# Kernel optimization log

Hardware: AMD Instinct MI355X
Metric: run time of the kernel (lower is better)

Reference implementation:

```python
import jax, jax.numpy as jnp
import numpy as np

LOG_SQRT_2PI = 0.5 * float(np.log(2.0 * np.pi))  # 0.5*log(2*pi)


def _bayes_layer(x, mu, p, eps):
    # std_w = 1e-6 + softplus(W_p); W = W_mu + std_w * eps
    std = 1e-6 + jax.nn.softplus(p)
    W = mu + std * eps
    out = x @ W
    # variational posterior loglike q(W | mu, std), summed
    lqw = jnp.sum(-LOG_SQRT_2PI - jnp.log(std) - 0.5 * ((W - mu) / std) ** 2)
    # prior loglike N(0, 1) on detached W (original does W.detach().cpu().numpy())
    Wd = jax.lax.stop_gradient(W)
    lpw = jnp.sum(-LOG_SQRT_2PI - 0.5 * Wd ** 2)
    return out, lqw, lpw


def setup_inputs() -> dict:
    key = jax.random.key(0)
    ks = jax.random.split(key, 10)
    B, D_in, D_h, D_out = 65536, 512, 512, 10
    u = lambda k, s, lo, hi: jax.random.uniform(k, s, jnp.float32, lo, hi)
    return {
        "x": jax.random.normal(ks[0], (B, D_in), jnp.float32),
        "W_mu1": u(ks[1], (D_in, D_h), -0.2, 0.2),
        "W_p1": u(ks[2], (D_in, D_h), -3.0, -2.0),
        "eps1": jax.random.normal(ks[3], (D_in, D_h), jnp.float32),
        "W_mu2": u(ks[4], (D_h, D_h), -0.2, 0.2),
        "W_p2": u(ks[5], (D_h, D_h), -3.0, -2.0),
        "eps2": jax.random.normal(ks[6], (D_h, D_h), jnp.float32),
        "W_mu3": u(ks[7], (D_h, D_out), -0.2, 0.2),
        "W_p3": u(ks[8], (D_h, D_out), -3.0, -2.0),
        "eps3": jax.random.normal(ks[9], (D_h, D_out), jnp.float32),
    }


def reference(x, W_mu1, W_p1, eps1, W_mu2, W_p2, eps2, W_mu3, W_p3, eps3):
    # training / sample=True path of bayes_linear_2L.forward
    h, lqw1, lpw1 = _bayes_layer(x, W_mu1, W_p1, eps1)
    h = jax.nn.relu(h)
    h, lqw2, lpw2 = _bayes_layer(h, W_mu2, W_p2, eps2)
    h = jax.nn.relu(h)
    y, lqw3, lpw3 = _bayes_layer(h, W_mu3, W_p3, eps3)
    tlqw = lqw1 + lqw2 + lqw3
    tlpw = lpw1 + lpw2 + lpw3
    return (y, tlqw, tlpw)
```

## Files before the change

kernel.cpp:

```cpp
#include <hip/hip_runtime.h>
#include <hip/hip_bf16.h>
#include <stdint.h>

typedef unsigned char u8;
typedef unsigned int u32;
typedef unsigned long long u64;
typedef long i64;
typedef i64 i64x2 __attribute__((ext_vector_type(2)));
typedef float f32x4 __attribute__((ext_vector_type(4)));

#define LOGSQRT2PI 0.9189385332046727f
#define SB0() __builtin_amdgcn_sched_barrier(0)
#define MFMA8(A, B, C) __builtin_amdgcn_mfma_f32_16x16x32_fp8_fp8(A, B, C, 0, 0, 0)

__device__ __forceinline__ void gload_lds16(const void* g, void* l) {
    __builtin_amdgcn_global_load_lds((__attribute__((address_space(1))) void*)g,
                                     (__attribute__((address_space(3))) void*)l,
                                     16, 0, 0);
}

__device__ __forceinline__ u8 to_fp8(float v) {
    return (u8)(__builtin_amdgcn_cvt_pk_fp8_f32(v, 0.f, 0, false) & 0xff);
}

__device__ __forceinline__ i64x2 cvt_frag(const float* base) {
    float4 v0 = *(const float4*)(base);
    float4 v1 = *(const float4*)(base + 4);
    float4 v2 = *(const float4*)(base + 8);
    float4 v3 = *(const float4*)(base + 12);
    u32 w0 = __builtin_amdgcn_cvt_pk_fp8_f32(v0.x, v0.y, 0, false);
    w0 = __builtin_amdgcn_cvt_pk_fp8_f32(v0.z, v0.w, (int)w0, true);
    u32 w1 = __builtin_amdgcn_cvt_pk_fp8_f32(v1.x, v1.y, 0, false);
    w1 = __builtin_amdgcn_cvt_pk_fp8_f32(v1.z, v1.w, (int)w1, true);
    u32 w2 = __builtin_amdgcn_cvt_pk_fp8_f32(v2.x, v2.y, 0, false);
    w2 = __builtin_amdgcn_cvt_pk_fp8_f32(v2.z, v2.w, (int)w2, true);
    u32 w3 = __builtin_amdgcn_cvt_pk_fp8_f32(v3.x, v3.y, 0, false);
    w3 = __builtin_amdgcn_cvt_pk_fp8_f32(v3.z, v3.w, (int)w3, true);
    i64x2 rr;
    rr.x = (i64)(((u64)w1 << 32) | (u64)w0);
    rr.y = (i64)(((u64)w3 << 32) | (u64)w2);
    return rr;
}

__device__ __forceinline__ void prep_body(const float* __restrict__ mu,
        const float* __restrict__ p, const float* __restrict__ eps,
        u8* __restrict__ Wt, int N, int Npad, float* __restrict__ osc,
        int vb, int nblocks) {
    int total = 512 * Npad;
    float lqw = 0.f, lpw = 0.f;
    for (int idx = vb * 256 + threadIdx.x; idx < total; idx += nblocks * 256) {
        int k = idx / Npad, n = idx - k * Npad;
        float w = 0.f;
        if (n < N) {
            int src = k * N + n;
            float m = mu[src], e = eps[src];
            float sd = 1e-6f + log1pf(expf(p[src]));
            w = m + sd * e;
            float z = (w - m) / sd;
            lqw += -LOGSQRT2PI - logf(sd) - 0.5f * z * z;
            lpw += -LOGSQRT2PI - 0.5f * w * w;
        }
        Wt[n * 512 + k] = to_fp8(w);
    }
    #pragma unroll
    for (int off = 32; off; off >>= 1) {
        lqw += __shfl_down(lqw, off);
        lpw += __shfl_down(lpw, off);
    }
    if ((threadIdx.x & 63) == 0) {
        atomicAdd(&osc[0], lqw);
        atomicAdd(&osc[1], lpw);
    }
}

__global__ void k_prep_all(const float* __restrict__ mu1, const float* __restrict__ p1,
                           const float* __restrict__ e1,
                           const float* __restrict__ mu2, const float* __restrict__ p2,
                           const float* __restrict__ e2,
                           const float* __restrict__ mu3, const float* __restrict__ p3,
                           const float* __restrict__ e3,
                           u8* __restrict__ Wt1, u8* __restrict__ Wt2,
                           u8* __restrict__ Wt3, float* __restrict__ osc) {
    int b = blockIdx.x;
    if (b < 256)      prep_body(mu1, p1, e1, Wt1, 512, 512, osc, b, 256);
    else if (b < 512) prep_body(mu2, p2, e2, Wt2, 512, 512, osc, b - 256, 256);
    else              prep_body(mu3, p3, e3, Wt3, 10,  16,  osc, b - 512, 16);
}

__global__ __launch_bounds__(256, 2)
void k_f8(const float* __restrict__ X, const u8* __restrict__ W1t,
          const u8* __restrict__ W2t, const u8* __restrict__ W3t,
          float* __restrict__ Y) {
    __shared__ __align__(16) u8 L[81920];
    const int tid = threadIdx.x;
    const int l = tid & 63, w = tid >> 6;
    const int r = l & 15, kq = l >> 4;
    const int l16 = l * 16;
    const long m0 = (long)blockIdx.x * 128 + w * 32;
    u8* scr = &L[65536 + w * 4096];

    #define STAGEW(WT, NT, BUF) { _Pragma("unroll")                            \
        for (int i = 0; i < 8; i++) {                                          \
            const int c = w * 8 + i;                                           \
            const int jg = c & 3, kt = c >> 2;                                 \
            gload_lds16((WT) + ((NT) * 64 + jg * 16 + r) * 512 + kt * 64 + kq * 16, \
                        &L[(BUF) * 32768 + c * 1024 + l16]);                   \
        } }

    #define GLOOP(BUF, XA, XB) { _Pragma("unroll")                             \
        for (int kt = 0; kt < 8; kt++)                                         \
            _Pragma("unroll")                                                  \
            for (int jg = 0; jg < 4; jg++) {                                   \
                i64x2 bfr = *(const i64x2*)&L[(BUF) * 32768 + (kt * 4 + jg) * 1024 + l16]; \
                accA[jg] = MFMA8(XA[kt].x, bfr.x, accA[jg]);                   \
                accA[jg] = MFMA8(XA[kt].y, bfr.y, accA[jg]);                   \
                accB[jg] = MFMA8(XB[kt].x, bfr.x, accB[jg]);                   \
                accB[jg] = MFMA8(XB[kt].y, bfr.y, accB[jg]);                   \
            } }

    #define TOSCR() { _Pragma("unroll")                                        \
        for (int jg = 0; jg < 4; jg++)                                         \
            _Pragma("unroll")                                                  \
            for (int q = 0; q < 4; q++) {                                      \
                int rowA = kq * 4 + q;                                         \
                int rowB = 16 + kq * 4 + q;                                    \
                scr[rowA * 128 + ((jg ^ (rowA & 7)) << 4) + r] =               \
                    to_fp8(fmaxf(accA[jg][q], 0.f));                           \
                scr[rowB * 128 + ((jg ^ (rowB & 7)) << 4) + r] =               \
                    to_fp8(fmaxf(accB[jg][q], 0.f));                           \
            } }

    #define ZACC() { _Pragma("unroll")                                         \
        for (int jg = 0; jg < 4; jg++) {                                       \
            accA[jg] = (f32x4){0.f, 0.f, 0.f, 0.f};                            \
            accB[jg] = (f32x4){0.f, 0.f, 0.f, 0.f};                            \
        } }

    f32x4 accA[4], accB[4];
    i64x2 xfA[8], xfB[8];
    i64x2 h1fA[8], h1fB[8];
    f32x4 yA = (f32x4){0.f, 0.f, 0.f, 0.f};
    f32x4 yB = (f32x4){0.f, 0.f, 0.f, 0.f};

    STAGEW(W1t, 0, 0);
    #pragma unroll
    for (int kt = 0; kt < 8; kt++) {
        xfA[kt] = cvt_frag(X + (m0 + r) * 512 + kt * 64 + kq * 16);
        xfB[kt] = cvt_frag(X + (m0 + 16 + r) * 512 + kt * 64 + kq * 16);
    }
    asm volatile("s_waitcnt vmcnt(0)" ::: "memory");
    __builtin_amdgcn_s_barrier();

    #pragma unroll 1
    for (int nt = 0; nt < 8; nt++) {
        const int buf = nt & 1;
        if (nt < 7) { STAGEW(W1t, nt + 1, buf ^ 1); }
        else        { STAGEW(W2t, 0, buf ^ 1); }
        ZACC();
        GLOOP(buf, xfA, xfB);
        TOSCR();
        asm volatile("s_waitcnt lgkmcnt(0)" ::: "memory");
        SB0();
        h1fA[nt] = *(const i64x2*)&scr[r * 128 + ((kq ^ (r & 7)) << 4)];
        h1fB[nt] = *(const i64x2*)&scr[(16 + r) * 128 + ((kq ^ (r & 7)) << 4)];
        asm volatile("s_waitcnt lgkmcnt(0)" ::: "memory");
        SB0();
        asm volatile("s_waitcnt vmcnt(0)" ::: "memory");
        __builtin_amdgcn_s_barrier();
    }

    #pragma unroll 1
    for (int nt = 0; nt < 8; nt++) {
        const int buf = (nt + 1) & 1;
        if (nt < 7) STAGEW(W2t, nt + 1, buf ^ 1);
        ZACC();
        GLOOP(buf, h1fA, h1fB);
        TOSCR();
        asm volatile("s_waitcnt lgkmcnt(0)" ::: "memory");
        SB0();
        {
            i64x2 a3A = *(const i64x2*)&scr[r * 128 + ((kq ^ (r & 7)) << 4)];
            i64x2 a3B = *(const i64x2*)&scr[(16 + r) * 128 + ((kq ^ (r & 7)) << 4)];
            i64x2 w3 = *(const i64x2*)(W3t + r * 512 + nt * 64 + kq * 16);
            yA = MFMA8(a3A.x, w3.x, yA);
            yA = MFMA8(a3A.y, w3.y, yA);
            yB = MFMA8(a3B.x, w3.x, yB);
            yB = MFMA8(a3B.y, w3.y, yB);
        }
        asm volatile("s_waitcnt lgkmcnt(0)" ::: "memory");
        SB0();
        if (nt < 7) { asm volatile("s_waitcnt vmcnt(0)" ::: "memory"); }
        __builtin_amdgcn_s_barrier();
    }

    if (r < 10) {
        #pragma unroll
        for (int q = 0; q < 4; q++) {
            Y[(m0 + kq * 4 + q) * 10 + r]      = yA[q];
            Y[(m0 + 16 + kq * 4 + q) * 10 + r] = yB[q];
        }
    }
    #undef STAGEW
    #undef GLOOP
    #undef TOSCR
    #undef ZACC
}

extern "C" void kernel_launch(void* const* d_in, const int* in_sizes, int n_in,
                              void* d_out, int out_size, void* d_ws, size_t ws_size,
                              hipStream_t stream) {
    const float* x   = (const float*)d_in[0];
    const float* mu1 = (const float*)d_in[1];
    const float* p1  = (const float*)d_in[2];
    const float* e1  = (const float*)d_in[3];
    const float* mu2 = (const float*)d_in[4];
    const float* p2  = (const float*)d_in[5];
    const float* e2  = (const float*)d_in[6];
    const float* mu3 = (const float*)d_in[7];
    const float* p3  = (const float*)d_in[8];
    const float* e3  = (const float*)d_in[9];
    float* out = (float*)d_out;

    const int B = 65536, DO = 10;

    char* ws = (char*)d_ws;
    u8* Wt1 = (u8*)(ws);
    u8* Wt2 = (u8*)(ws + 262144);
    u8* Wt3 = (u8*)(ws + 524288);

    float* osc = out + (long)B * DO;

    hipMemsetAsync(osc, 0, 2 * sizeof(float), stream);
    hipLaunchKernelGGL(k_prep_all, dim3(528), dim3(256), 0, stream,
                       mu1, p1, e1, mu2, p2, e2, mu3, p3, e3, Wt1, Wt2, Wt3, osc);
    hipLaunchKernelGGL(k_f8, dim3(512), dim3(256), 0, stream,
                       x, Wt1, Wt2, Wt3, out);
}
```

Before: 138.4 us.

## Split layer-1 by row half to overlap X loading with MFMA compute

Layer 1 is split into two passes, first over rows A and then over rows B. The fp32 X loads for the B half are issued while the A-half MFMA loops run, so global reads of X overlap compute instead of all landing in the prologue. The change also raises MFMA wave priority with s_setprio around the inner loops and doubles the prep kernel's grid. In exchange, W1 is now streamed through LDS twice with twice as many barriers, and the in-flight float4 buffers raise register pressure.

```diff
diff --git a/kernel.cpp b/kernel.cpp
--- a/kernel.cpp
+++ b/kernel.cpp
@@ -23,19 +23,15 @@
     return (u8)(__builtin_amdgcn_cvt_pk_fp8_f32(v, 0.f, 0, false) & 0xff);
 }
 
-__device__ __forceinline__ i64x2 cvt_frag(const float* base) {
-    float4 v0 = *(const float4*)(base);
-    float4 v1 = *(const float4*)(base + 4);
-    float4 v2 = *(const float4*)(base + 8);
-    float4 v3 = *(const float4*)(base + 12);
-    u32 w0 = __builtin_amdgcn_cvt_pk_fp8_f32(v0.x, v0.y, 0, false);
-    w0 = __builtin_amdgcn_cvt_pk_fp8_f32(v0.z, v0.w, (int)w0, true);
-    u32 w1 = __builtin_amdgcn_cvt_pk_fp8_f32(v1.x, v1.y, 0, false);
-    w1 = __builtin_amdgcn_cvt_pk_fp8_f32(v1.z, v1.w, (int)w1, true);
-    u32 w2 = __builtin_amdgcn_cvt_pk_fp8_f32(v2.x, v2.y, 0, false);
-    w2 = __builtin_amdgcn_cvt_pk_fp8_f32(v2.z, v2.w, (int)w2, true);
-    u32 w3 = __builtin_amdgcn_cvt_pk_fp8_f32(v3.x, v3.y, 0, false);
-    w3 = __builtin_amdgcn_cvt_pk_fp8_f32(v3.z, v3.w, (int)w3, true);
+__device__ __forceinline__ i64x2 pack_frag(const float4* v) {
+    u32 w0 = __builtin_amdgcn_cvt_pk_fp8_f32(v[0].x, v[0].y, 0, false);
+    w0 = __builtin_amdgcn_cvt_pk_fp8_f32(v[0].z, v[0].w, (int)w0, true);
+    u32 w1 = __builtin_amdgcn_cvt_pk_fp8_f32(v[1].x, v[1].y, 0, false);
+    w1 = __builtin_amdgcn_cvt_pk_fp8_f32(v[1].z, v[1].w, (int)w1, true);
+    u32 w2 = __builtin_amdgcn_cvt_pk_fp8_f32(v[2].x, v[2].y, 0, false);
+    w2 = __builtin_amdgcn_cvt_pk_fp8_f32(v[2].z, v[2].w, (int)w2, true);
+    u32 w3 = __builtin_amdgcn_cvt_pk_fp8_f32(v[3].x, v[3].y, 0, false);
+    w3 = __builtin_amdgcn_cvt_pk_fp8_f32(v[3].z, v[3].w, (int)w3, true);
     i64x2 rr;
     rr.x = (i64)(((u64)w1 << 32) | (u64)w0);
     rr.y = (i64)(((u64)w3 << 32) | (u64)w2);
@@ -82,9 +78,9 @@
                            u8* __restrict__ Wt1, u8* __restrict__ Wt2,
                            u8* __restrict__ Wt3, float* __restrict__ osc) {
     int b = blockIdx.x;
-    if (b < 256)      prep_body(mu1, p1, e1, Wt1, 512, 512, osc, b, 256);
-    else if (b < 512) prep_body(mu2, p2, e2, Wt2, 512, 512, osc, b - 256, 256);
-    else              prep_body(mu3, p3, e3, Wt3, 10,  16,  osc, b - 512, 16);
+    if (b < 512)       prep_body(mu1, p1, e1, Wt1, 512, 512, osc, b, 512);
+    else if (b < 1024) prep_body(mu2, p2, e2, Wt2, 512, 512, osc, b - 512, 512);
+    else               prep_body(mu3, p3, e3, Wt3, 10,  16,  osc, b - 1024, 16);
 }
 
 __global__ __launch_bounds__(256, 2)
@@ -107,77 +103,122 @@
                         &L[(BUF) * 32768 + c * 1024 + l16]);                   \
         } }
 
-    #define GLOOP(BUF, XA, XB) { _Pragma("unroll")                             \
-        for (int kt = 0; kt < 8; kt++)                                         \
-            _Pragma("unroll")                                                  \
-            for (int jg = 0; jg < 4; jg++) {                                   \
-                i64x2 bfr = *(const i64x2*)&L[(BUF) * 32768 + (kt * 4 + jg) * 1024 + l16]; \
-                accA[jg] = MFMA8(XA[kt].x, bfr.x, accA[jg]);                   \
-                accA[jg] = MFMA8(XA[kt].y, bfr.y, accA[jg]);                   \
-                accB[jg] = MFMA8(XB[kt].x, bfr.x, accB[jg]);                   \
-                accB[jg] = MFMA8(XB[kt].y, bfr.y, accB[jg]);                   \
-            } }
-
-    #define TOSCR() { _Pragma("unroll")                                        \
-        for (int jg = 0; jg < 4; jg++)                                         \
-            _Pragma("unroll")                                                  \
-            for (int q = 0; q < 4; q++) {                                      \
-                int rowA = kq * 4 + q;                                         \
-                int rowB = 16 + kq * 4 + q;                                    \
-                scr[rowA * 128 + ((jg ^ (rowA & 7)) << 4) + r] =               \
-                    to_fp8(fmaxf(accA[jg][q], 0.f));                           \
-                scr[rowB * 128 + ((jg ^ (rowB & 7)) << 4) + r] =               \
-                    to_fp8(fmaxf(accB[jg][q], 0.f));                           \
-            } }
-
-    #define ZACC() { _Pragma("unroll")                                         \
-        for (int jg = 0; jg < 4; jg++) {                                       \
-            accA[jg] = (f32x4){0.f, 0.f, 0.f, 0.f};                            \
-            accB[jg] = (f32x4){0.f, 0.f, 0.f, 0.f};                            \
-        } }
-
     f32x4 accA[4], accB[4];
     i64x2 xfA[8], xfB[8];
     i64x2 h1fA[8], h1fB[8];
     f32x4 yA = (f32x4){0.f, 0.f, 0.f, 0.f};
     f32x4 yB = (f32x4){0.f, 0.f, 0.f, 0.f};
 
+    const float* xrowA = X + (m0 + r) * 512 + kq * 16;
+    const float* xrowB = X + (m0 + 16 + r) * 512 + kq * 16;
+
     STAGEW(W1t, 0, 0);
-    #pragma unroll
-    for (int kt = 0; kt < 8; kt++) {
-        xfA[kt] = cvt_frag(X + (m0 + r) * 512 + kt * 64 + kq * 16);
-        xfB[kt] = cvt_frag(X + (m0 + 16 + r) * 512 + kt * 64 + kq * 16);
+    {
+        float4 q0[16], q1[16];
+        #pragma unroll
+        for (int f = 0; f < 4; f++)
+            #pragma unroll
+            for (int o = 0; o < 4; o++) {
+                q0[f * 4 + o] = *(const float4*)(xrowA + f * 64 + o * 4);
+                q1[f * 4 + o] = *(const float4*)(xrowA + (4 + f) * 64 + o * 4);
+            }
+        #pragma unroll
+        for (int f = 0; f < 4; f++) {
+            xfA[f]     = pack_frag(&q0[f * 4]);
+            xfA[4 + f] = pack_frag(&q1[f * 4]);
+        }
     }
     asm volatile("s_waitcnt vmcnt(0)" ::: "memory");
     __builtin_amdgcn_s_barrier();
 
+    auto phase1 = [&](int nt, const i64x2* xf, i64x2* hf, f32x4* acc,
+                      const u8* Wthis, const u8* Wnext) {
+        const int buf = nt & 1;
+        if (nt < 7) { STAGEW(Wthis, nt + 1, buf ^ 1); }
+        else        { STAGEW(Wnext, 0, buf ^ 1); }
+        #pragma unroll
+        for (int jg = 0; jg < 4; jg++) acc[jg] = (f32x4){0.f, 0.f, 0.f, 0.f};
+        __builtin_amdgcn_s_setprio(1);
+        #pragma unroll
+        for (int kt = 0; kt < 8; kt++)
+            #pragma unroll
+            for (int jg = 0; jg < 4; jg++) {
+                i64x2 bfr = *(const i64x2*)&L[buf * 32768 + (kt * 4 + jg) * 1024 + l16];
+                acc[jg] = MFMA8(xf[kt].x, bfr.x, acc[jg]);
+                acc[jg] = MFMA8(xf[kt].y, bfr.y, acc[jg]);
+            }
+        __builtin_amdgcn_s_setprio(0);
+        #pragma unroll
+        for (int jg = 0; jg < 4; jg++)
+            #pragma unroll
+            for (int q = 0; q < 4; q++) {
+                int row = kq * 4 + q;
+                scr[row * 128 + ((jg ^ (row & 7)) << 4) + r] =
+                    to_fp8(fmaxf(acc[jg][q], 0.f));
+            }
+        asm volatile("s_waitcnt lgkmcnt(0)" ::: "memory"); SB0();
+        hf[nt] = *(const i64x2*)&scr[r * 128 + ((kq ^ (r & 7)) << 4)];
+        asm volatile("s_waitcnt lgkmcnt(0)" ::: "memory"); SB0();
+        asm volatile("s_waitcnt vmcnt(0)" ::: "memory");
+        __builtin_amdgcn_s_barrier();
+    };
+
+    float4 qB[16];
+    #pragma unroll
+    for (int f = 0; f < 4; f++)
+        #pragma unroll
+        for (int o = 0; o < 4; o++)
+            qB[f * 4 + o] = *(const float4*)(xrowB + f * 64 + o * 4);
+    #pragma unroll 1
+    for (int nt = 0; nt < 4; nt++) phase1(nt, xfA, h1fA, accA, W1t, W1t);
+    #pragma unroll
+    for (int f = 0; f < 4; f++) xfB[f] = pack_frag(&qB[f * 4]);
+    #pragma unroll
+    for (int f = 0; f < 4; f++)
+        #pragma unroll
+        for (int o = 0; o < 4; o++)
+            qB[f * 4 + o] = *(const float4*)(xrowB + (4 + f) * 64 + o * 4);
+    #pragma unroll 1
+    for (int nt = 4; nt < 8; nt++) phase1(nt, xfA, h1fA, accA, W1t, W1t);
+    #pragma unroll
+    for (int f = 0; f < 4; f++) xfB[4 + f] = pack_frag(&qB[f * 4]);
+
+    #pragma unroll 1
+    for (int nt = 0; nt < 8; nt++) phase1(nt, xfB, h1fB, accA, W1t, W2t);
+
     #pragma unroll 1
     for (int nt = 0; nt < 8; nt++) {
         const int buf = nt & 1;
-        if (nt < 7) { STAGEW(W1t, nt + 1, buf ^ 1); }
-        else        { STAGEW(W2t, 0, buf ^ 1); }
-        ZACC();
-        GLOOP(buf, xfA, xfB);
-        TOSCR();
-        asm volatile("s_waitcnt lgkmcnt(0)" ::: "memory");
-        SB0();
-        h1fA[nt] = *(const i64x2*)&scr[r * 128 + ((kq ^ (r & 7)) << 4)];
-        h1fB[nt] = *(const i64x2*)&scr[(16 + r) * 128 + ((kq ^ (r & 7)) << 4)];
-        asm volatile("s_waitcnt lgkmcnt(0)" ::: "memory");
-        SB0();
-        asm volatile("s_waitcnt vmcnt(0)" ::: "memory");
-        __builtin_amdgcn_s_barrier();
-    }
-
-    #pragma unroll 1
-    for (int nt = 0; nt < 8; nt++) {
-        const int buf = (nt + 1) & 1;
         if (nt < 7) STAGEW(W2t, nt + 1, buf ^ 1);
-        ZACC();
-        GLOOP(buf, h1fA, h1fB);
-        TOSCR();
-        asm volatile("s_waitcnt lgkmcnt(0)" ::: "memory");
-        SB0();
+        #pragma unroll
+        for (int jg = 0; jg < 4; jg++) {
+            accA[jg] = (f32x4){0.f, 0.f, 0.f, 0.f};
+            accB[jg] = (f32x4){0.f, 0.f, 0.f, 0.f};
+        }
+        __builtin_amdgcn_s_setprio(1);
+        #pragma unroll
+        for (int kt = 0; kt < 8; kt++)
+            #pragma unroll
+            for (int jg = 0; jg < 4; jg++) {
+                i64x2 bfr = *(const i64x2*)&L[buf * 32768 + (kt * 4 + jg) * 1024 + l16];
+                accA[jg] = MFMA8(h1fA[kt].x, bfr.x, accA[jg]);
+                accA[jg] = MFMA8(h1fA[kt].y, bfr.y, accA[jg]);
+                accB[jg] = MFMA8(h1fB[kt].x, bfr.x, accB[jg]);
+                accB[jg] = MFMA8(h1fB[kt].y, bfr.y, accB[jg]);
+            }
+        __builtin_amdgcn_s_setprio(0);
+        #pragma unroll
+        for (int jg = 0; jg < 4; jg++)
+            #pragma unroll
+            for (int q = 0; q < 4; q++) {
+                int rowA = kq * 4 + q;
+                int rowB = 16 + kq * 4 + q;
+                scr[rowA * 128 + ((jg ^ (rowA & 7)) << 4) + r] =
+                    to_fp8(fmaxf(accA[jg][q], 0.f));
+                scr[rowB * 128 + ((jg ^ (rowB & 7)) << 4) + r] =
+                    to_fp8(fmaxf(accB[jg][q], 0.f));
+            }
+        asm volatile("s_waitcnt lgkmcnt(0)" ::: "memory"); SB0();
         {
             i64x2 a3A = *(const i64x2*)&scr[r * 128 + ((kq ^ (r & 7)) << 4)];
             i64x2 a3B = *(const i64x2*)&scr[(16 + r) * 128 + ((kq ^ (r & 7)) << 4)];
@@ -187,8 +228,7 @@
             yB = MFMA8(a3B.x, w3.x, yB);
             yB = MFMA8(a3B.y, w3.y, yB);
         }
-        asm volatile("s_waitcnt lgkmcnt(0)" ::: "memory");
-        SB0();
+        asm volatile("s_waitcnt lgkmcnt(0)" ::: "memory"); SB0();
         if (nt < 7) { asm volatile("s_waitcnt vmcnt(0)" ::: "memory"); }
         __builtin_amdgcn_s_barrier();
     }
@@ -201,9 +241,6 @@
         }
     }
     #undef STAGEW
-    #undef GLOOP
-    #undef TOSCR
-    #undef ZACC
 }
 
 extern "C" void kernel_launch(void* const* d_in, const int* in_sizes, int n_in,
@@ -231,7 +268,7 @@
     float* osc = out + (long)B * DO;
 
     hipMemsetAsync(osc, 0, 2 * sizeof(float), stream);
-    hipLaunchKernelGGL(k_prep_all, dim3(528), dim3(256), 0, stream,
+    hipLaunchKernelGGL(k_prep_all, dim3(1040), dim3(256), 0, stream,
                        mu1, p1, e1, mu2, p2, e2, mu3, p3, e3, Wt1, Wt2, Wt3, osc);
     hipLaunchKernelGGL(k_f8, dim3(512), dim3(256), 0, stream,
                        x, Wt1, Wt2, Wt3, out);
```

After: 203.9 us. 1.47x slower.
